# Kernel tuning notes

Measured on AMD Instinct MI355X. Metric: run time of the kernel, lower is better.

Reference implementation:

```python
import jax, jax.numpy as jnp
import numpy as np

B, S, H, T = 64, 512, 768, 9


def setup_inputs() -> dict:
    key = jax.random.key(0)
    ks = jax.random.split(key, 8)
    embeddings = jax.random.normal(ks[0], (B, S, H), dtype=jnp.float32)
    # variable-length mask (first token always valid), as token_type_ids would give
    lengths = jax.random.randint(ks[1], (B,), 1, S + 1)
    mask = (jnp.arange(S)[None, :] < lengths[:, None]).astype(jnp.int32)
    labels = jax.random.randint(ks[2], (B, S), 0, T)
    W = jax.random.normal(ks[3], (T, H), dtype=jnp.float32) * (1.0 / np.sqrt(H))
    b = jnp.zeros((T,), dtype=jnp.float32)
    start_trans = jax.random.normal(ks[4], (T,), dtype=jnp.float32) * 0.1
    transitions = jax.random.normal(ks[5], (T, T), dtype=jnp.float32) * 0.1
    end_trans = jax.random.normal(ks[6], (T,), dtype=jnp.float32) * 0.1
    return {"embeddings": embeddings, "W": W, "b": b,
            "start_trans": start_trans, "transitions": transitions,
            "end_trans": end_trans, "labels": labels, "mask": mask}


def _crf_nll(emissions, labels, mask_bool, start_trans, transitions, end_trans):
    # emissions: [B,S,T]; returns negative log-likelihood per sequence [B]
    Bn = emissions.shape[0]
    mask_f = mask_bool.astype(emissions.dtype)
    # --- gold path score (numerator) ---
    first = start_trans[labels[:, 0]] + emissions[jnp.arange(Bn), 0, labels[:, 0]]
    emis_sc = jnp.take_along_axis(emissions, labels[..., None], axis=2)[..., 0]  # [B,S]
    trans_sc = transitions[labels[:, :-1], labels[:, 1:]]                         # [B,S-1]
    num = first + jnp.sum((emis_sc[:, 1:] + trans_sc) * mask_f[:, 1:], axis=1)
    last_idx = jnp.sum(mask_bool.astype(jnp.int32), axis=1) - 1
    last_lab = jnp.take_along_axis(labels, last_idx[:, None], axis=1)[:, 0]
    num = num + end_trans[last_lab]
    # --- log partition (forward algorithm, logsumexp recurrence) ---
    alpha0 = start_trans[None, :] + emissions[:, 0]          # [B,T]
    em_t = jnp.swapaxes(emissions, 0, 1)[1:]                 # [S-1,B,T]
    m_t = mask_bool.T[1:]                                    # [S-1,B]
    def step(alpha, xs):
        em, m = xs
        new = jax.nn.logsumexp(alpha[:, :, None] + transitions[None], axis=1) + em
        return jnp.where(m[:, None], new, alpha), None
    alpha, _ = jax.lax.scan(step, alpha0, (em_t, m_t))
    denom = jax.nn.logsumexp(alpha + end_trans[None, :], axis=1)
    return denom - num


def reference(embeddings, W, b, start_trans, transitions, end_trans, labels, mask):
    # dropout is identity at eval; Linear + ReLU emissions
    emissions = jax.nn.relu(jnp.einsum('bsh,th->bst', embeddings, W) + b)
    # -100 padding handling: zero out mask there, clamp labels to 0
    valid = labels != -100
    mask_bool = (mask != 0) & valid
    labels_mod = jnp.where(valid, labels, 0)
    nll = _crf_nll(emissions, labels_mod, mask_bool, start_trans, transitions, end_trans)
    return jnp.mean(nll)  # == -loss.mean() of the log-likelihood
```

## Files before the change

kernel.cpp:

```cpp
#include <hip/hip_runtime.h>

#define NEG_INF (-1e30f)

static constexpr int Bn = 64;
static constexpr int Sn = 512;
static constexpr int Hn = 768;
static constexpr int Tn = 9;
static constexpr int KC = 32;
static constexpr int PSTRIDE = 108;

typedef __attribute__((ext_vector_type(8))) short short8;
typedef __attribute__((ext_vector_type(4))) float f32x4;

__device__ __forceinline__ short f2bf(float x) {
    __bf16 h = (__bf16)x;
    return __builtin_bit_cast(short, h);
}

__device__ __forceinline__ short8 pack_bf16x8(float4 a, float4 b) {
    short8 r;
    r[0] = f2bf(a.x); r[1] = f2bf(a.y); r[2] = f2bf(a.z); r[3] = f2bf(a.w);
    r[4] = f2bf(b.x); r[5] = f2bf(b.y); r[6] = f2bf(b.z); r[7] = f2bf(b.w);
    return r;
}

__global__ __launch_bounds__(512, 4) void fused_kernel(
        const float* __restrict__ emb, const float* __restrict__ Wm,
        const float* __restrict__ bias, const float* __restrict__ trans,
        const int* __restrict__ labels, const int* __restrict__ mask,
        float* __restrict__ chunkP, float* __restrict__ auxN,
        int* __restrict__ auxC, float* __restrict__ emRow0) {
    const int blk  = blockIdx.x;
    const int tid  = threadIdx.x;
    const int lane = tid & 63;
    const int wv   = tid >> 6;
    const int tile = wv & 3;
    const int kh   = wv >> 2;

    __shared__ float emH[2][64][10];
    __shared__ float em_s[64][10];
    __shared__ float tr_s[81];

    if (tid < 81) tr_s[tid] = trans[tid];

    const int t9 = lane & 15;
    const int kg = lane >> 4;

    short8 wf[12];
    {
        const float* wrow = Wm + t9 * Hn + kh * 384 + kg * 8;
#pragma unroll
        for (int s = 0; s < 12; ++s) {
            if (t9 < Tn) {
                float4 w0 = *(const float4*)(wrow + s * 32);
                float4 w1 = *(const float4*)(wrow + s * 32 + 4);
                wf[s] = pack_bf16x8(w0, w1);
            } else {
                short8 z = {0, 0, 0, 0, 0, 0, 0, 0};
                wf[s] = z;
            }
        }
    }

    const int rowBase = blk * 64;
    const float* arow = emb + (size_t)(rowBase + tile * 16 + t9) * Hn
                        + kh * 384 + kg * 8;
    float4 pf0[4], pf1[4];
#pragma unroll
    for (int d = 0; d < 4; ++d) {
        pf0[d] = *(const float4*)(arow + d * 32);
        pf1[d] = *(const float4*)(arow + d * 32 + 4);
    }
    f32x4 acc = {0.0f, 0.0f, 0.0f, 0.0f};
#pragma unroll
    for (int s = 0; s < 12; ++s) {
        float4 a0 = pf0[s & 3];
        float4 a1 = pf1[s & 3];
        if (s + 4 < 12) {
            pf0[s & 3] = *(const float4*)(arow + (s + 4) * 32);
            pf1[s & 3] = *(const float4*)(arow + (s + 4) * 32 + 4);
        }
        short8 af = pack_bf16x8(a0, a1);
        acc = __builtin_amdgcn_mfma_f32_16x16x32_bf16(af, wf[s], acc, 0, 0, 0);
    }

    if (t9 < Tn) {
#pragma unroll
        for (int r = 0; r < 4; ++r)
            emH[kh][tile * 16 + kg * 4 + r][t9] = acc[r];
    }
    __syncthreads();

    for (int o = tid; o < 64 * Tn; o += 512) {
        int r = o / Tn, t = o - r * Tn;
        float v = fmaxf(emH[0][r][t] + emH[1][r][t] + bias[t], 0.0f);
        em_s[r][t] = v;
        if ((blk & 7) == 0 && r == 0) emRow0[(blk >> 3) * Tn + t] = v;
    }
    __syncthreads();

    const int h  = wv & 1;
    const int cl = wv >> 1;
    const int b  = blk >> 3;
    const int sc = (blk & 7) * 4 + cl;
    const int s0 = (blk & 7) * 64;

    const int u16 = lane & 15;
    const int tstep = s0 + cl * 16 + u16;
    int lb = 0, on = 0;
    if (lane < 16) {
        lb = labels[b * Sn + tstep];
        int mm = mask[b * Sn + tstep];
        on = (tstep >= 1) && (mm != 0) && (lb != -100);
    }
    unsigned long long bm = __ballot(on != 0);

    if (h == 0) {
        float np = 0.0f;
        int c1 = 0;
        if (lane < 16 && on) {
            int lpr = labels[b * Sn + tstep - 1];
            lpr = (lpr == -100) ? 0 : lpr;
            np = em_s[cl * 16 + u16][lb] + tr_s[lpr * Tn + lb];
            c1 = 1;
        }
#pragma unroll
        for (int off = 8; off; off >>= 1) {
            np += __shfl_xor(np, off);
            c1 += __shfl_xor(c1, off);
        }
        if (lane == 0) { auxN[b * KC + sc] = np; auxC[b * KC + sc] = c1; }
    }

    const int v  = lane / 9;
    const int jj = lane - v * 9;
    const bool act = lane < (h ? 36 : 45);
    const int rid = h ? (5 + v) : v;

    float c[Tn];
#pragma unroll
    for (int kk = 0; kk < Tn; ++kk) c[kk] = tr_s[kk * Tn + jj];

    float pv = (act && rid == jj) ? 0.0f : NEG_INF;

    for (int u = 0; u < 16; ++u) {
        if (!((bm >> u) & 1ull)) continue;
        float x[Tn];
#pragma unroll
        for (int kk = 0; kk < Tn; ++kk) {
            float a = __shfl(pv, (v * Tn + kk) & 63);
            x[kk] = a + c[kk];
        }
        float mx = x[0];
#pragma unroll
        for (int kk = 1; kk < Tn; ++kk) mx = fmaxf(mx, x[kk]);
        float s = 0.0f;
#pragma unroll
        for (int kk = 0; kk < Tn; ++kk) s += __expf(x[kk] - mx);
        float nv = mx + __logf(s) + em_s[cl * 16 + u][jj];
        pv = act ? nv : pv;
    }
    if (act) chunkP[(size_t)(b * KC + sc) * PSTRIDE + jj * 12 + rid] = pv;
}

__global__ __launch_bounds__(64) void combine_kernel(
        const float* __restrict__ emRow0, const float* __restrict__ startT,
        const float* __restrict__ endT, const int* __restrict__ labels,
        const int* __restrict__ mask, const float* __restrict__ chunkP,
        const float* __restrict__ auxN, const int* __restrict__ auxC,
        float* __restrict__ nll) {
    const int b = blockIdx.x;
    const int lane = threadIdx.x;

    float em0 = (lane < Tn) ? emRow0[b * Tn + lane] : NEG_INF;
    float alpha = (lane < Tn) ? (startT[lane] + em0) : NEG_INF;

    int lab0r = labels[b * Sn];
    int lab0 = (lab0r == -100) ? 0 : lab0r;
    float first = startT[lab0] + __shfl(em0, lab0);

    float numP = (lane < KC) ? auxN[b * KC + lane] : 0.0f;
    int   cntP = (lane < KC) ? auxC[b * KC + lane] : 0;
#pragma unroll
    for (int off = 32; off; off >>= 1) {
        numP += __shfl_xor(numP, off);
        cntP += __shfl_xor(cntP, off);
    }
    int m0 = ((mask[b * Sn] != 0) && (lab0r != -100)) ? 1 : 0;
    int cntTot = cntP + m0;
    int lastIdx = cntTot - 1;
    if (lastIdx < 0) lastIdx = 0;
    int lastLab = labels[b * Sn + lastIdx];
    lastLab = (lastLab == -100) ? 0 : lastLab;
    float num = first + numP + endT[lastLab];

    const float* Pb = chunkP + (size_t)b * KC * PSTRIDE;
    float4 p0 = make_float4(0, 0, 0, 0), p1 = p0, p2 = p0;
    if (lane < Tn) {
        const float4* pp = (const float4*)(Pb + lane * 12);
        p0 = pp[0]; p1 = pp[1]; p2 = pp[2];
    }
    for (int k = 0; k < KC; ++k) {
        float4 q0 = p0, q1 = p1, q2 = p2;
        if (k + 1 < KC && lane < Tn) {
            const float4* pp = (const float4*)(Pb + (size_t)(k + 1) * PSTRIDE + lane * 12);
            p0 = pp[0]; p1 = pp[1]; p2 = pp[2];
        }
        float av[Tn];
#pragma unroll
        for (int i = 0; i < Tn; ++i) av[i] = __shfl(alpha, i);
        float x[Tn];
        x[0] = av[0] + q0.x; x[1] = av[1] + q0.y; x[2] = av[2] + q0.z;
        x[3] = av[3] + q0.w; x[4] = av[4] + q1.x; x[5] = av[5] + q1.y;
        x[6] = av[6] + q1.z; x[7] = av[7] + q1.w; x[8] = av[8] + q2.x;
        float mx = x[0];
#pragma unroll
        for (int i = 1; i < Tn; ++i) mx = fmaxf(mx, x[i]);
        float s = 0.0f;
#pragma unroll
        for (int i = 0; i < Tn; ++i) s += __expf(x[i] - mx);
        float na = mx + __logf(s);
        alpha = (lane < Tn) ? na : NEG_INF;
    }

    float z = (lane < Tn) ? (alpha + endT[lane]) : NEG_INF;
    float mx = z;
#pragma unroll
    for (int off = 32; off; off >>= 1) mx = fmaxf(mx, __shfl_xor(mx, off));
    float s = __expf(z - mx);
#pragma unroll
    for (int off = 32; off; off >>= 1) s += __shfl_xor(s, off);
    float denom = mx + __logf(s);

    if (lane == 0) nll[b] = denom - num;
}

__global__ __launch_bounds__(64) void mean_kernel(const float* __restrict__ nll,
        float* __restrict__ out) {
    float v = nll[threadIdx.x];
#pragma unroll
    for (int off = 32; off; off >>= 1) v += __shfl_xor(v, off);
    if (threadIdx.x == 0) out[0] = v * (1.0f / 64.0f);
}

extern "C" void kernel_launch(void* const* d_in, const int* in_sizes, int n_in,
                              void* d_out, int out_size, void* d_ws, size_t ws_size,
                              hipStream_t stream) {
    const float* emb    = (const float*)d_in[0];
    const float* Wm     = (const float*)d_in[1];
    const float* bias   = (const float*)d_in[2];
    const float* startT = (const float*)d_in[3];
    const float* trans  = (const float*)d_in[4];
    const float* endT   = (const float*)d_in[5];
    const int*   labels = (const int*)d_in[6];
    const int*   mask   = (const int*)d_in[7];

    float* chunkP = (float*)d_ws;
    float* auxN   = chunkP + (size_t)Bn * KC * PSTRIDE;
    int*   auxC   = (int*)(auxN + (size_t)Bn * KC);
    float* nll    = (float*)(auxC + (size_t)Bn * KC);
    float* emRow0 = nll + Bn;
    float* out    = (float*)d_out;

    fused_kernel<<<512, 512, 0, stream>>>(emb, Wm, bias, trans, labels, mask,
                                          chunkP, auxN, auxC, emRow0);
    combine_kernel<<<Bn, 64, 0, stream>>>(emRow0, startT, endT, labels, mask,
                                          chunkP, auxN, auxC, nll);
    mean_kernel<<<1, 64, 0, stream>>>(nll, out);
}
```

Measured before the change: 55.93 us.

## Stage embedding tiles through LDS via global_load_lds with smaller 32-row blocks

```diff
diff --git a/kernel.cpp b/kernel.cpp
--- a/kernel.cpp
+++ b/kernel.cpp
@@ -8,6 +8,8 @@
 static constexpr int Tn = 9;
 static constexpr int KC = 32;
 static constexpr int PSTRIDE = 108;
+static constexpr int RB = 32;
+static constexpr int BK = 128;
 
 typedef __attribute__((ext_vector_type(8))) short short8;
 typedef __attribute__((ext_vector_type(4))) float f32x4;
@@ -24,7 +26,13 @@
     return r;
 }
 
-__global__ __launch_bounds__(512, 4) void fused_kernel(
+__device__ __forceinline__ void gll16(const float* g, float* l) {
+    __builtin_amdgcn_global_load_lds(
+        (const __attribute__((address_space(1))) void*)g,
+        (__attribute__((address_space(3))) void*)l, 16, 0, 0);
+}
+
+__global__ __launch_bounds__(256, 4) void fused_kernel(
         const float* __restrict__ emb, const float* __restrict__ Wm,
         const float* __restrict__ bias, const float* __restrict__ trans,
         const int* __restrict__ labels, const int* __restrict__ mask,
@@ -34,11 +42,12 @@
     const int tid  = threadIdx.x;
     const int lane = tid & 63;
     const int wv   = tid >> 6;
-    const int tile = wv & 3;
-    const int kh   = wv >> 2;
-
-    __shared__ float emH[2][64][10];
-    __shared__ float em_s[64][10];
+    const int tl   = wv & 1;
+    const int kh   = wv >> 1;
+
+    __shared__ float Ast[RB * BK];
+    __shared__ float emH[2][RB][10];
+    __shared__ float em_s[RB][10];
     __shared__ float tr_s[81];
 
     if (tid < 81) tr_s[tid] = trans[tid];
@@ -47,63 +56,71 @@
     const int kg = lane >> 4;
 
     short8 wf[12];
-    {
-        const float* wrow = Wm + t9 * Hn + kh * 384 + kg * 8;
-#pragma unroll
-        for (int s = 0; s < 12; ++s) {
+#pragma unroll
+    for (int s = 0; s < 6; ++s) {
+#pragma unroll
+        for (int m = 0; m < 2; ++m) {
             if (t9 < Tn) {
-                float4 w0 = *(const float4*)(wrow + s * 32);
-                float4 w1 = *(const float4*)(wrow + s * 32 + 4);
-                wf[s] = pack_bf16x8(w0, w1);
+                const float* wp = Wm + t9 * Hn + s * 128 + kh * 64 + m * 32 + kg * 8;
+                float4 w0 = *(const float4*)wp;
+                float4 w1 = *(const float4*)(wp + 4);
+                wf[s * 2 + m] = pack_bf16x8(w0, w1);
             } else {
                 short8 z = {0, 0, 0, 0, 0, 0, 0, 0};
-                wf[s] = z;
+                wf[s * 2 + m] = z;
             }
         }
     }
 
-    const int rowBase = blk * 64;
-    const float* arow = emb + (size_t)(rowBase + tile * 16 + t9) * Hn
-                        + kh * 384 + kg * 8;
-    float4 pf0[4], pf1[4];
-#pragma unroll
-    for (int d = 0; d < 4; ++d) {
-        pf0[d] = *(const float4*)(arow + d * 32);
-        pf1[d] = *(const float4*)(arow + d * 32 + 4);
-    }
+    int goff[4];
+#pragma unroll
+    for (int j = 0; j < 4; ++j) {
+        int L = tid + j * 256;
+        int r = L >> 5, ls = L & 31;
+        goff[j] = r * Hn + ((ls ^ (r & 7)) << 2);
+    }
+    const float* gbase = emb + (size_t)blk * RB * Hn;
+
+    const int rA   = tl * 16 + t9;
+    const int rx   = rA & 7;
     f32x4 acc = {0.0f, 0.0f, 0.0f, 0.0f};
-#pragma unroll
-    for (int s = 0; s < 12; ++s) {
-        float4 a0 = pf0[s & 3];
-        float4 a1 = pf1[s & 3];
-        if (s + 4 < 12) {
-            pf0[s & 3] = *(const float4*)(arow + (s + 4) * 32);
-            pf1[s & 3] = *(const float4*)(arow + (s + 4) * 32 + 4);
-        }
-        short8 af = pack_bf16x8(a0, a1);
-        acc = __builtin_amdgcn_mfma_f32_16x16x32_bf16(af, wf[s], acc, 0, 0, 0);
+    for (int s = 0; s < 6; ++s) {
+        if (s) __syncthreads();
+#pragma unroll
+        for (int j = 0; j < 4; ++j)
+            gll16(gbase + goff[j] + s * BK, &Ast[(j * 256 + wv * 64) * 4]);
+        asm volatile("s_waitcnt vmcnt(0)" ::: "memory");
+        __syncthreads();
+#pragma unroll
+        for (int m = 0; m < 2; ++m) {
+            int c4 = kh * 16 + m * 8 + kg * 2;
+            float4 a0 = *(const float4*)&Ast[(rA * 32 + (c4 ^ rx)) * 4];
+            float4 a1 = *(const float4*)&Ast[(rA * 32 + ((c4 + 1) ^ rx)) * 4];
+            short8 af = pack_bf16x8(a0, a1);
+            acc = __builtin_amdgcn_mfma_f32_16x16x32_bf16(af, wf[s * 2 + m], acc, 0, 0, 0);
+        }
     }
 
     if (t9 < Tn) {
 #pragma unroll
         for (int r = 0; r < 4; ++r)
-            emH[kh][tile * 16 + kg * 4 + r][t9] = acc[r];
+            emH[kh][tl * 16 + kg * 4 + r][t9] = acc[r];
     }
     __syncthreads();
 
-    for (int o = tid; o < 64 * Tn; o += 512) {
+    for (int o = tid; o < RB * Tn; o += 256) {
         int r = o / Tn, t = o - r * Tn;
         float v = fmaxf(emH[0][r][t] + emH[1][r][t] + bias[t], 0.0f);
         em_s[r][t] = v;
-        if ((blk & 7) == 0 && r == 0) emRow0[(blk >> 3) * Tn + t] = v;
+        if ((blk & 15) == 0 && r == 0) emRow0[(blk >> 4) * Tn + t] = v;
     }
     __syncthreads();
 
     const int h  = wv & 1;
     const int cl = wv >> 1;
-    const int b  = blk >> 3;
-    const int sc = (blk & 7) * 4 + cl;
-    const int s0 = (blk & 7) * 64;
+    const int b  = blk >> 4;
+    const int sc = (blk & 15) * 2 + cl;
+    const int s0 = (blk & 15) * 32;
 
     const int u16 = lane & 15;
     const int tstep = s0 + cl * 16 + u16;
@@ -262,8 +279,9 @@
     float* emRow0 = nll + Bn;
     float* out    = (float*)d_out;
 
-    fused_kernel<<<512, 512, 0, stream>>>(emb, Wm, bias, trans, labels, mask,
-                                          chunkP, auxN, auxC, emRow0);
+    fused_kernel<<<Bn * Sn / RB, 256, 0, stream>>>(emb, Wm, bias, trans,
+                                                   labels, mask, chunkP,
+                                                   auxN, auxC, emRow0);
     combine_kernel<<<Bn, 64, 0, stream>>>(emRow0, startT, endT, labels, mask,
                                           chunkP, auxN, auxC, nll);
     mean_kernel<<<1, 64, 0, stream>>>(nll, out);
```

Result: no change. 55.69 us (-0.4%).
